# Kernel optimization log

Hardware: AMD Instinct MI355X
Metric: run time of the kernel (lower is better)

## Reference

```python
import jax, jax.numpy as jnp
import numpy as np

K = 16      # knn neighbors (init kwarg k)
EPS = 1e-5  # batch-norm eps


def setup_inputs() -> dict:
    key = jax.random.key(0)
    ks = jax.random.split(key, 4)
    B, N, C, O = 16, 2048, 16, 64
    x = jax.random.normal(ks[0], (B * N, C), dtype=jnp.float32)
    batch = jnp.repeat(jnp.arange(B, dtype=jnp.int32), N)  # sorted equal-size graphs
    W1 = jax.random.normal(ks[1], (2 * C, O), dtype=jnp.float32) * (1.0 / np.sqrt(2 * C))
    b1 = jnp.zeros((O,), jnp.float32)
    g1 = jnp.ones((O,), jnp.float32)
    be1 = jnp.zeros((O,), jnp.float32)
    Wg = jax.random.normal(ks[2], (O, 1), dtype=jnp.float32) * (1.0 / np.sqrt(O))
    bg = jnp.zeros((1,), jnp.float32)
    gg = jnp.ones((1,), jnp.float32)
    beg = jnp.zeros((1,), jnp.float32)
    return {"x": x, "batch": batch, "W1": W1, "b1": b1, "g1": g1, "be1": be1,
            "Wg": Wg, "bg": bg, "gg": gg, "beg": beg, "num_graphs": B}


def reference(x, batch, W1, b1, g1, be1, Wg, bg, gg, beg, num_graphs):
    B = int(num_graphs)
    total, C = x.shape
    N = total // B
    xb = x.reshape(B, N, C)

    # --- dynamic kNN graph in feature space (per graph in the batch) ---
    sq = jnp.sum(xb * xb, axis=-1)                                   # [B,N]
    d = sq[:, :, None] + sq[:, None, :] - 2.0 * jnp.einsum('bnc,bmc->bnm', xb, xb)
    _, idx = jax.lax.top_k(-d, K)                                    # [B,N,K], includes self (d=0)

    # --- edge features: cat([x_i, x_j - x_i]) ---
    xj = jax.vmap(lambda pts, ids: pts[ids])(xb, idx)                # [B,N,K,C]
    xi = jnp.broadcast_to(xb[:, :, None, :], xj.shape)               # [B,N,K,C]
    e = jnp.concatenate([xi, xj - xi], axis=-1)                      # [B,N,K,2C]

    # --- edge MLP: Linear -> BatchNorm(train stats) -> SiLU ---
    h = e @ W1 + b1                                                  # [B,N,K,O]
    mu = h.mean(axis=(0, 1, 2))
    var = h.var(axis=(0, 1, 2))
    h = jax.nn.silu((h - mu) / jnp.sqrt(var + EPS) * g1 + be1)

    # --- attentional aggregation: gate MLP -> softmax over k edges -> weighted sum ---
    gt = h @ Wg + bg                                                 # [B,N,K,1]
    gmu = gt.mean()
    gvar = gt.var()
    gt = jax.nn.silu((gt - gmu) / jnp.sqrt(gvar + EPS) * gg + beg)
    a = jax.nn.softmax(gt, axis=2)                                   # softmax over K per target node
    out = jnp.sum(a * h, axis=2)                                     # [B,N,O]
    return out.reshape(total, -1)
```

## Files before the change

kernel.cpp:

```cpp
#include <hip/hip_runtime.h>
#include <math.h>
#include <float.h>

#define BGRAPH 16
#define NPTS   2048
#define CDIM   16
#define ODIM   64
#define KNN    16
#define NTOT   (BGRAPH*NPTS)
#define NEDGE  (NTOT*KNN)
#define EPSBN  1e-5f
#define NBLK_E 2048
#define NPW    4

__global__ __launch_bounds__(256) void pq_kernel(
    const float* __restrict__ x, const float* __restrict__ W1,
    const float* __restrict__ b1,
    float* __restrict__ P, float* __restrict__ Q, float* __restrict__ sq) {
  int lane = threadIdx.x & 63;
  int nin  = threadIdx.x >> 6;
  int node = blockIdx.x * 4 + nin;
  __shared__ float xs[4][CDIM];
  if (threadIdx.x < 4*CDIM) {
    int n = threadIdx.x / CDIM, c = threadIdx.x % CDIM;
    xs[n][c] = x[(blockIdx.x*4 + n)*CDIM + c];
  }
  __syncthreads();
  float p = 0.f, q = b1[lane];
  #pragma unroll
  for (int c = 0; c < CDIM; ++c) {
    float xv = xs[nin][c];
    float wb = W1[(c+CDIM)*ODIM + lane];
    float wa = W1[c*ODIM + lane];
    p += xv * wb;
    q += xv * (wa - wb);
  }
  P[node*ODIM + lane] = p;
  Q[node*ODIM + lane] = q;
  if (lane == 0) {
    float s = 0.f;
    #pragma unroll
    for (int c = 0; c < CDIM; ++c) { float xv = xs[nin][c]; s += xv*xv; }
    sq[node] = s;
  }
}

#define KROWS 4
__device__ __forceinline__ unsigned long long packkey(float dv, int j) {
  unsigned ub = __float_as_uint(dv);
  ub ^= ((unsigned)((int)ub >> 31)) | 0x80000000u;
  return (((unsigned long long)ub) << 32) | (unsigned)j;
}

__global__ __launch_bounds__(256, 4) void knn_kernel(
    const float* __restrict__ x, const float* __restrict__ sq,
    int* __restrict__ idxOut) {
  __shared__ float sT16[CDIM][256];
  __shared__ unsigned long long skey[4][64];
  __shared__ int scnt[4];
  const int tid  = threadIdx.x;
  const int lane = tid & 63;
  const int w    = tid >> 6;
  const int blocksPerGraph = NPTS / KROWS;
  const int g     = blockIdx.x / blocksPerGraph;
  const int rb    = (blockIdx.x % blocksPerGraph) * KROWS;
  const int gbase = g * NPTS;
  const int r0    = rb + w;

  float tg[CDIM]; float tsq;
  {
    const float4* tp = (const float4*)(x + (size_t)(gbase + r0)*CDIM);
    float4 t0 = tp[0], t1 = tp[1], t2 = tp[2], t3 = tp[3];
    tg[0]=t0.x; tg[1]=t0.y; tg[2]=t0.z; tg[3]=t0.w;
    tg[4]=t1.x; tg[5]=t1.y; tg[6]=t1.z; tg[7]=t1.w;
    tg[8]=t2.x; tg[9]=t2.y; tg[10]=t2.z; tg[11]=t2.w;
    tg[12]=t3.x; tg[13]=t3.y; tg[14]=t3.z; tg[15]=t3.w;
    tsq = sq[gbase + r0];
  }

  float d[32];

  float4 a0, a1, a2, a3;
  {
    const float4* xp = (const float4*)(x + (size_t)(gbase + tid)*CDIM);
    a0 = xp[0]; a1 = xp[1]; a2 = xp[2]; a3 = xp[3];
  }

  for (int t = 0; t < NPTS/256; ++t) {
    __syncthreads();
    sT16[0][tid]=a0.x;  sT16[1][tid]=a0.y;  sT16[2][tid]=a0.z;  sT16[3][tid]=a0.w;
    sT16[4][tid]=a1.x;  sT16[5][tid]=a1.y;  sT16[6][tid]=a1.z;  sT16[7][tid]=a1.w;
    sT16[8][tid]=a2.x;  sT16[9][tid]=a2.y;  sT16[10][tid]=a2.z; sT16[11][tid]=a2.w;
    sT16[12][tid]=a3.x; sT16[13][tid]=a3.y; sT16[14][tid]=a3.z; sT16[15][tid]=a3.w;
    __syncthreads();
    if (t < NPTS/256 - 1) {
      const float4* xp = (const float4*)(x + (size_t)(gbase + (t+1)*256 + tid)*CDIM);
      a0 = xp[0]; a1 = xp[1]; a2 = xp[2]; a3 = xp[3];
    }

    float4 sq4 = *(const float4*)(sq + gbase + t*256 + 4*lane);
    float sqv[4] = {sq4.x, sq4.y, sq4.z, sq4.w};

    float dot[4] = {0.f,0.f,0.f,0.f};
    #pragma unroll
    for (int c = 0; c < CDIM; ++c) {
      float4 cv = *(const float4*)(&sT16[c][4*lane]);
      float cvv[4]; cvv[0]=cv.x; cvv[1]=cv.y; cvv[2]=cv.z; cvv[3]=cv.w;
      float xv = tg[c];
      #pragma unroll
      for (int rr = 0; rr < 4; ++rr)
        dot[rr] += xv * cvv[rr];
    }
    #pragma unroll
    for (int rr = 0; rr < 4; ++rr)
      d[t*4 + rr] = tsq + sqv[rr] - 2.f*dot[rr];
  }

  {
    float lmin = d[0];
    #pragma unroll
    for (int s = 1; s < 32; ++s) lmin = fminf(lmin, d[s]);

    float v = lmin;
    #pragma unroll
    for (int k = 2; k <= 64; k <<= 1) {
      #pragma unroll
      for (int j = k >> 1; j > 0; j >>= 1) {
        float o = __shfl_xor(v, j);
        bool asc   = ((lane & k) == 0);
        bool lower = ((lane & j) == 0);
        float mn = fminf(v, o), mx = fmaxf(v, o);
        v = (asc == lower) ? mn : mx;
      }
    }
    float T = __shfl(v, 15);

    if (lane == 0) scnt[w] = 0;
    #pragma unroll
    for (int s = 0; s < 32; ++s) {
      if (d[s] <= T) {
        int p = atomicAdd(&scnt[w], 1);
        if (p < 64) {
          int j = (s >> 2)*256 + 4*lane + (s & 3);
          skey[w][p] = packkey(d[s], j);
        }
      }
    }
    int M = scnt[w];
    int row = gbase + r0;

    if (M <= 64) {
      unsigned long long key = (lane < M) ? skey[w][lane] : ~0ull;
      #pragma unroll
      for (int k = 2; k <= 64; k <<= 1) {
        #pragma unroll
        for (int j = k >> 1; j > 0; j >>= 1) {
          unsigned long long o = __shfl_xor(key, j);
          bool asc   = ((lane & k) == 0);
          bool lower = ((lane & j) == 0);
          unsigned long long mn = (key < o) ? key : o;
          unsigned long long mx = (key < o) ? o : key;
          key = (asc == lower) ? mn : mx;
        }
      }
      if (lane < KNN)
        idxOut[(size_t)row*KNN + lane] = gbase + (int)(key & 0xffffffffu);
    } else {
      for (int sel = 0; sel < KNN; ++sel) {
        unsigned long long lb = ~0ull;
        #pragma unroll
        for (int s = 0; s < 32; ++s) {
          int j = (s >> 2)*256 + 4*lane + (s & 3);
          unsigned long long ks = packkey(d[s], j);
          if (ks < lb) lb = ks;
        }
        #pragma unroll
        for (int off = 32; off > 0; off >>= 1) {
          unsigned long long o = __shfl_xor(lb, off);
          if (o < lb) lb = o;
        }
        if (lane == 0)
          idxOut[(size_t)row*KNN + sel] = gbase + (int)(lb & 0xffffffffu);
        #pragma unroll
        for (int s = 0; s < 32; ++s) {
          int j = (s >> 2)*256 + 4*lane + (s & 3);
          if (packkey(d[s], j) == lb) d[s] = FLT_MAX;
        }
      }
    }
  }
}

__global__ __launch_bounds__(256) void stats1_kernel(
    const float* __restrict__ P, const float* __restrict__ Q,
    const int* __restrict__ idx, float* __restrict__ pbuf) {
  int lane = threadIdx.x & 63;
  int wid  = threadIdx.x >> 6;
  int grp  = lane >> 4;
  int p    = lane & 15;
  int gw   = blockIdx.x * 4 + wid;
  int n0 = gw * NPW;
  float4 s4  = {0.f,0.f,0.f,0.f};
  float4 ss4 = {0.f,0.f,0.f,0.f};
  #pragma unroll
  for (int ii = 0; ii < NPW; ++ii) {
    int i = n0 + ii;
    float4 q4 = *(const float4*)(Q + (size_t)i*ODIM + 4*p);
    int4 j4 = *(const int4*)(idx + (size_t)i*KNN + 4*grp);
    {
      float4 v = *(const float4*)(P + (size_t)j4.x*ODIM + 4*p);
      float hx=q4.x+v.x, hy=q4.y+v.y, hz=q4.z+v.z, hw=q4.w+v.w;
      s4.x+=hx; s4.y+=hy; s4.z+=hz; s4.w+=hw;
      ss4.x+=hx*hx; ss4.y+=hy*hy; ss4.z+=hz*hz; ss4.w+=hw*hw;
    }
    {
      float4 v = *(const float4*)(P + (size_t)j4.y*ODIM + 4*p);
      float hx=q4.x+v.x, hy=q4.y+v.y, hz=q4.z+v.z, hw=q4.w+v.w;
      s4.x+=hx; s4.y+=hy; s4.z+=hz; s4.w+=hw;
      ss4.x+=hx*hx; ss4.y+=hy*hy; ss4.z+=hz*hz; ss4.w+=hw*hw;
    }
    {
      float4 v = *(const float4*)(P + (size_t)j4.z*ODIM + 4*p);
      float hx=q4.x+v.x, hy=q4.y+v.y, hz=q4.z+v.z, hw=q4.w+v.w;
      s4.x+=hx; s4.y+=hy; s4.z+=hz; s4.w+=hw;
      ss4.x+=hx*hx; ss4.y+=hy*hy; ss4.z+=hz*hz; ss4.w+=hw*hw;
    }
    {
      float4 v = *(const float4*)(P + (size_t)j4.w*ODIM + 4*p);
      float hx=q4.x+v.x, hy=q4.y+v.y, hz=q4.z+v.z, hw=q4.w+v.w;
      s4.x+=hx; s4.y+=hy; s4.z+=hz; s4.w+=hw;
      ss4.x+=hx*hx; ss4.y+=hy*hy; ss4.z+=hz*hz; ss4.w+=hw*hw;
    }
  }
  s4.x  += __shfl_xor(s4.x,16);  s4.x  += __shfl_xor(s4.x,32);
  s4.y  += __shfl_xor(s4.y,16);  s4.y  += __shfl_xor(s4.y,32);
  s4.z  += __shfl_xor(s4.z,16);  s4.z  += __shfl_xor(s4.z,32);
  s4.w  += __shfl_xor(s4.w,16);  s4.w  += __shfl_xor(s4.w,32);
  ss4.x += __shfl_xor(ss4.x,16); ss4.x += __shfl_xor(ss4.x,32);
  ss4.y += __shfl_xor(ss4.y,16); ss4.y += __shfl_xor(ss4.y,32);
  ss4.z += __shfl_xor(ss4.z,16); ss4.z += __shfl_xor(ss4.z,32);
  ss4.w += __shfl_xor(ss4.w,16); ss4.w += __shfl_xor(ss4.w,32);
  __shared__ float ls[4][ODIM], lss[4][ODIM];
  if (grp == 0) {
    *(float4*)&ls[wid][4*p]  = s4;
    *(float4*)&lss[wid][4*p] = ss4;
  }
  __syncthreads();
  int tid = threadIdx.x;
  if (tid < ODIM) {
    float a = ls[0][tid] + ls[1][tid] + ls[2][tid] + ls[3][tid];
    pbuf[(size_t)tid*NBLK_E + blockIdx.x] = a;
  } else if (tid < 2*ODIM) {
    int o = tid - ODIM;
    float a = lss[0][o] + lss[1][o] + lss[2][o] + lss[3][o];
    pbuf[(size_t)(ODIM+o)*NBLK_E + blockIdx.x] = a;
  }
}

__global__ __launch_bounds__(64) void fin1_kernel(
    const float* __restrict__ pbuf,
    const float* __restrict__ g1, const float* __restrict__ be1,
    float* __restrict__ scale, float* __restrict__ shift) {
  int o = blockIdx.x, lane = threadIdx.x;
  const float* ps = pbuf + (size_t)o*NBLK_E;
  const float* pq = pbuf + (size_t)(ODIM+o)*NBLK_E;
  float s = 0.f, ss = 0.f;
  for (int t = lane; t < NBLK_E; t += 64) { s += ps[t]; ss += pq[t]; }
  #pragma unroll
  for (int off = 32; off > 0; off >>= 1) {
    s  += __shfl_xor(s, off);
    ss += __shfl_xor(ss, off);
  }
  if (lane == 0) {
    float mu  = s / (float)NEDGE;
    float var = ss / (float)NEDGE - mu*mu;
    float inv = 1.0f / sqrtf(var + EPSBN);
    float sc = g1[o] * inv;
    scale[o] = sc;
    shift[o] = be1[o] - mu * sc;
  }
}

__global__ __launch_bounds__(256) void stats2_kernel(
    const float* __restrict__ P, const float* __restrict__ Q,
    const int* __restrict__ idx, const float* __restrict__ scale,
    const float* __restrict__ shift, const float* __restrict__ Wg,
    const float* __restrict__ bg, float* __restrict__ gtbuf,
    float* __restrict__ gpart) {
  int lane = threadIdx.x & 63;
  int wid  = threadIdx.x >> 6;
  int grp  = lane >> 4;
  int p    = lane & 15;
  int gw   = blockIdx.x * 4 + wid;
  int n0 = gw * NPW;
  float4 sc4 = *(const float4*)(scale + 4*p);
  float4 sh4 = *(const float4*)(shift + 4*p);
  float4 wg4 = *(const float4*)(Wg + 4*p);
  float bgv = bg[0];
  float s = 0.f, ss = 0.f;
  #pragma unroll
  for (int ii = 0; ii < NPW; ++ii) {
    int i = n0 + ii;
    float4 q4 = *(const float4*)(Q + (size_t)i*ODIM + 4*p);
    int4 j4 = *(const int4*)(idx + (size_t)i*KNN + 4*grp);
    #pragma unroll
    for (int e = 0; e < 4; ++e) {
      int j = (e==0) ? j4.x : (e==1) ? j4.y : (e==2) ? j4.z : j4.w;
      float4 p4 = *(const float4*)(P + (size_t)j*ODIM + 4*p);
      float zx = (q4.x + p4.x)*sc4.x + sh4.x;
      float zy = (q4.y + p4.y)*sc4.y + sh4.y;
      float zz = (q4.z + p4.z)*sc4.z + sh4.z;
      float zw = (q4.w + p4.w)*sc4.w + sh4.w;
      float v = (zx/(1.f+expf(-zx)))*wg4.x
              + (zy/(1.f+expf(-zy)))*wg4.y
              + (zz/(1.f+expf(-zz)))*wg4.z
              + (zw/(1.f+expf(-zw)))*wg4.w;
      v += __shfl_xor(v, 1);
      v += __shfl_xor(v, 2);
      v += __shfl_xor(v, 4);
      v += __shfl_xor(v, 8);
      float gt = v + bgv;
      if (p == 0) gtbuf[(size_t)i*KNN + 4*grp + e] = gt;
      s += gt; ss += gt*gt;
    }
  }
  s  += __shfl_xor(s, 16);  s  += __shfl_xor(s, 32);
  ss += __shfl_xor(ss, 16); ss += __shfl_xor(ss, 32);
  __shared__ float pw[4], pws[4];
  if (lane == 0) { pw[wid] = s; pws[wid] = ss; }
  __syncthreads();
  if (threadIdx.x == 0) {
    gpart[2*blockIdx.x]   = pw[0]+pw[1]+pw[2]+pw[3];
    gpart[2*blockIdx.x+1] = pws[0]+pws[1]+pws[2]+pws[3];
  }
}

__global__ __launch_bounds__(256) void fin2_kernel(
    const float* __restrict__ gpart,
    const float* __restrict__ gg, const float* __restrict__ beg,
    float* __restrict__ gsc) {
  int tid = threadIdx.x;
  float s = 0.f, ss = 0.f;
  for (int t = tid; t < NBLK_E; t += 256) { s += gpart[2*t]; ss += gpart[2*t+1]; }
  __shared__ float as[256], bs[256];
  as[tid] = s; bs[tid] = ss;
  __syncthreads();
  #pragma unroll
  for (int st = 128; st > 0; st >>= 1) {
    if (tid < st) { as[tid] += as[tid+st]; bs[tid] += bs[tid+st]; }
    __syncthreads();
  }
  if (tid == 0) {
    float mu  = as[0] / (float)NEDGE;
    float var = bs[0] / (float)NEDGE - mu*mu;
    float inv = 1.f / sqrtf(var + EPSBN);
    float sg = gg[0] * inv;
    gsc[0] = sg; gsc[1] = beg[0] - mu * sg;
  }
}

__global__ __launch_bounds__(256) void final_kernel(
    const float* __restrict__ P, const float* __restrict__ Q,
    const int* __restrict__ idx, const float* __restrict__ scale,
    const float* __restrict__ shift, const float* __restrict__ gtbuf,
    const float* __restrict__ gsc, float* __restrict__ out) {
  int lane = threadIdx.x & 63;
  int wid  = threadIdx.x >> 6;
  int grp  = lane >> 4;
  int p    = lane & 15;
  int i = blockIdx.x * 4 + wid;
  float4 sc4 = *(const float4*)(scale + 4*p);
  float4 sh4 = *(const float4*)(shift + 4*p);
  float gscale = gsc[0], gshift = gsc[1];
  float4 q4 = *(const float4*)(Q + (size_t)i*ODIM + 4*p);
  int4   j4 = *(const int4*)(idx + (size_t)i*KNN + 4*grp);
  float4 g4 = *(const float4*)(gtbuf + (size_t)i*KNN + 4*grp);

  float z0 = g4.x*gscale + gshift, z1 = g4.y*gscale + gshift;
  float z2 = g4.z*gscale + gshift, z3 = g4.w*gscale + gshift;
  float gt0 = z0/(1.f+expf(-z0)), gt1 = z1/(1.f+expf(-z1));
  float gt2 = z2/(1.f+expf(-z2)), gt3 = z3/(1.f+expf(-z3));
  float m = fmaxf(fmaxf(gt0, gt1), fmaxf(gt2, gt3));
  m = fmaxf(m, __shfl_xor(m, 16));
  m = fmaxf(m, __shfl_xor(m, 32));
  float e0 = expf(gt0-m), e1 = expf(gt1-m), e2 = expf(gt2-m), e3 = expf(gt3-m);
  float se = e0+e1+e2+e3;
  se += __shfl_xor(se, 16);
  se += __shfl_xor(se, 32);
  float invs = 1.f / se;
  float a0 = e0*invs, a1 = e1*invs, a2 = e2*invs, a3 = e3*invs;

  float4 acc = {0.f,0.f,0.f,0.f};
  {
    float4 v = *(const float4*)(P + (size_t)j4.x*ODIM + 4*p);
    float zx=(q4.x+v.x)*sc4.x+sh4.x, zy=(q4.y+v.y)*sc4.y+sh4.y;
    float zz=(q4.z+v.z)*sc4.z+sh4.z, zw=(q4.w+v.w)*sc4.w+sh4.w;
    acc.x += a0*(zx/(1.f+expf(-zx))); acc.y += a0*(zy/(1.f+expf(-zy)));
    acc.z += a0*(zz/(1.f+expf(-zz))); acc.w += a0*(zw/(1.f+expf(-zw)));
  }
  {
    float4 v = *(const float4*)(P + (size_t)j4.y*ODIM + 4*p);
    float zx=(q4.x+v.x)*sc4.x+sh4.x, zy=(q4.y+v.y)*sc4.y+sh4.y;
    float zz=(q4.z+v.z)*sc4.z+sh4.z, zw=(q4.w+v.w)*sc4.w+sh4.w;
    acc.x += a1*(zx/(1.f+expf(-zx))); acc.y += a1*(zy/(1.f+expf(-zy)));
    acc.z += a1*(zz/(1.f+expf(-zz))); acc.w += a1*(zw/(1.f+expf(-zw)));
  }
  {
    float4 v = *(const float4*)(P + (size_t)j4.z*ODIM + 4*p);
    float zx=(q4.x+v.x)*sc4.x+sh4.x, zy=(q4.y+v.y)*sc4.y+sh4.y;
    float zz=(q4.z+v.z)*sc4.z+sh4.z, zw=(q4.w+v.w)*sc4.w+sh4.w;
    acc.x += a2*(zx/(1.f+expf(-zx))); acc.y += a2*(zy/(1.f+expf(-zy)));
    acc.z += a2*(zz/(1.f+expf(-zz))); acc.w += a2*(zw/(1.f+expf(-zw)));
  }
  {
    float4 v = *(const float4*)(P + (size_t)j4.w*ODIM + 4*p);
    float zx=(q4.x+v.x)*sc4.x+sh4.x, zy=(q4.y+v.y)*sc4.y+sh4.y;
    float zz=(q4.z+v.z)*sc4.z+sh4.z, zw=(q4.w+v.w)*sc4.w+sh4.w;
    acc.x += a3*(zx/(1.f+expf(-zx))); acc.y += a3*(zy/(1.f+expf(-zy)));
    acc.z += a3*(zz/(1.f+expf(-zz))); acc.w += a3*(zw/(1.f+expf(-zw)));
  }
  acc.x += __shfl_xor(acc.x,16); acc.x += __shfl_xor(acc.x,32);
  acc.y += __shfl_xor(acc.y,16); acc.y += __shfl_xor(acc.y,32);
  acc.z += __shfl_xor(acc.z,16); acc.z += __shfl_xor(acc.z,32);
  acc.w += __shfl_xor(acc.w,16); acc.w += __shfl_xor(acc.w,32);
  if (grp == 0)
    *(float4*)(out + (size_t)i*ODIM + 4*p) = acc;
}

extern "C" void kernel_launch(void* const* d_in, const int* in_sizes, int n_in,
                              void* d_out, int out_size, void* d_ws, size_t ws_size,
                              hipStream_t stream) {
  const float* x   = (const float*)d_in[0];
  const float* W1  = (const float*)d_in[2];
  const float* b1  = (const float*)d_in[3];
  const float* g1  = (const float*)d_in[4];
  const float* be1 = (const float*)d_in[5];
  const float* Wg  = (const float*)d_in[6];
  const float* bg  = (const float*)d_in[7];
  const float* gg  = (const float*)d_in[8];
  const float* beg = (const float*)d_in[9];
  float* out = (float*)d_out;

  char* ws = (char*)d_ws;
  int*   idx   = (int*)  (ws);
  float* P     = (float*)(ws + 2097152);
  float* Q     = (float*)(ws + 10485760);
  float* sq    = (float*)(ws + 18874368);
  float* pbuf  = (float*)(ws + 19005440);
  float* gpart = (float*)(ws + 20054016);
  float* gtbuf = (float*)(ws + 20070400);
  float* scale = (float*)(ws + 22167552);
  float* shift = (float*)(ws + 22167808);
  float* gsc   = (float*)(ws + 22168064);

  pq_kernel<<<NTOT/4, 256, 0, stream>>>(x, W1, b1, P, Q, sq);
  knn_kernel<<<NTOT/KROWS, 256, 0, stream>>>(x, sq, idx);
  stats1_kernel<<<NBLK_E, 256, 0, stream>>>(P, Q, idx, pbuf);
  fin1_kernel<<<ODIM, 64, 0, stream>>>(pbuf, g1, be1, scale, shift);
  stats2_kernel<<<NBLK_E, 256, 0, stream>>>(P, Q, idx, scale, shift, Wg, bg, gtbuf, gpart);
  fin2_kernel<<<1, 256, 0, stream>>>(gpart, gg, beg, gsc);
  final_kernel<<<NTOT/4, 256, 0, stream>>>(P, Q, idx, scale, shift, gtbuf, gsc, out);
}
```

Baseline: 278.7 us.

## Fuse BN stats, gate and aggregation stages into one cooperative kernel with grid syncs

Replaces the five post-kNN launches (stats1, fin1, stats2, fin2, final) with a single cooperative kernel of 1024 blocks that separates the phases with grid.sync(). Each wave handles 8 nodes, and the per-block partial reductions and finalisations run inside the same kernel. The aim is to cut launch overhead and inter-kernel gaps. In exchange it adds grid-wide barrier costs and needs all 1024 blocks to be co-resident, falling back to the old launches if the cooperative launch fails.

```diff
diff --git a/kernel.cpp b/kernel.cpp
--- a/kernel.cpp
+++ b/kernel.cpp
@@ -1,6 +1,9 @@
 #include <hip/hip_runtime.h>
+#include <hip/hip_cooperative_groups.h>
 #include <math.h>
 #include <float.h>
+
+namespace cg = cooperative_groups;
 
 #define BGRAPH 16
 #define NPTS   2048
@@ -11,6 +14,7 @@
 #define NEDGE  (NTOT*KNN)
 #define EPSBN  1e-5f
 #define NBLK_E 2048
+#define NBLKF  1024
 #define NPW    4
 
 __global__ __launch_bounds__(256) void pq_kernel(
@@ -191,6 +195,234 @@
   }
 }
 
+__global__ __launch_bounds__(256, 4) void fused_kernel(
+    const float* __restrict__ P, const float* __restrict__ Q,
+    const int* __restrict__ idx,
+    const float* __restrict__ g1, const float* __restrict__ be1,
+    const float* __restrict__ Wg, const float* __restrict__ bg,
+    const float* __restrict__ gg, const float* __restrict__ beg,
+    float* __restrict__ pbuf, float* __restrict__ gpart,
+    float* __restrict__ gtbuf, float* __restrict__ scale,
+    float* __restrict__ shift, float* __restrict__ gsc,
+    float* __restrict__ out) {
+  cg::grid_group grid = cg::this_grid();
+  const int tid  = threadIdx.x;
+  const int lane = tid & 63;
+  const int wid  = tid >> 6;
+  const int grp  = lane >> 4;
+  const int p    = lane & 15;
+  const int blk  = blockIdx.x;
+  const int nw0  = blk*32 + wid*8;
+
+  __shared__ float ls[4][ODIM], lss[4][ODIM];
+  __shared__ float ra[256], rb[256];
+  __shared__ float pw[4], pws[4];
+
+  {
+    float4 s4 = {0.f,0.f,0.f,0.f};
+    float4 ss4 = {0.f,0.f,0.f,0.f};
+    for (int ii = 0; ii < 8; ++ii) {
+      int i = nw0 + ii;
+      float4 q4 = *(const float4*)(Q + (size_t)i*ODIM + 4*p);
+      int4 j4 = *(const int4*)(idx + (size_t)i*KNN + 4*grp);
+      {
+        float4 v = *(const float4*)(P + (size_t)j4.x*ODIM + 4*p);
+        float hx=q4.x+v.x, hy=q4.y+v.y, hz=q4.z+v.z, hw=q4.w+v.w;
+        s4.x+=hx; s4.y+=hy; s4.z+=hz; s4.w+=hw;
+        ss4.x+=hx*hx; ss4.y+=hy*hy; ss4.z+=hz*hz; ss4.w+=hw*hw;
+      }
+      {
+        float4 v = *(const float4*)(P + (size_t)j4.y*ODIM + 4*p);
+        float hx=q4.x+v.x, hy=q4.y+v.y, hz=q4.z+v.z, hw=q4.w+v.w;
+        s4.x+=hx; s4.y+=hy; s4.z+=hz; s4.w+=hw;
+        ss4.x+=hx*hx; ss4.y+=hy*hy; ss4.z+=hz*hz; ss4.w+=hw*hw;
+      }
+      {
+        float4 v = *(const float4*)(P + (size_t)j4.z*ODIM + 4*p);
+        float hx=q4.x+v.x, hy=q4.y+v.y, hz=q4.z+v.z, hw=q4.w+v.w;
+        s4.x+=hx; s4.y+=hy; s4.z+=hz; s4.w+=hw;
+        ss4.x+=hx*hx; ss4.y+=hy*hy; ss4.z+=hz*hz; ss4.w+=hw*hw;
+      }
+      {
+        float4 v = *(const float4*)(P + (size_t)j4.w*ODIM + 4*p);
+        float hx=q4.x+v.x, hy=q4.y+v.y, hz=q4.z+v.z, hw=q4.w+v.w;
+        s4.x+=hx; s4.y+=hy; s4.z+=hz; s4.w+=hw;
+        ss4.x+=hx*hx; ss4.y+=hy*hy; ss4.z+=hz*hz; ss4.w+=hw*hw;
+      }
+    }
+    s4.x  += __shfl_xor(s4.x,16);  s4.x  += __shfl_xor(s4.x,32);
+    s4.y  += __shfl_xor(s4.y,16);  s4.y  += __shfl_xor(s4.y,32);
+    s4.z  += __shfl_xor(s4.z,16);  s4.z  += __shfl_xor(s4.z,32);
+    s4.w  += __shfl_xor(s4.w,16);  s4.w  += __shfl_xor(s4.w,32);
+    ss4.x += __shfl_xor(ss4.x,16); ss4.x += __shfl_xor(ss4.x,32);
+    ss4.y += __shfl_xor(ss4.y,16); ss4.y += __shfl_xor(ss4.y,32);
+    ss4.z += __shfl_xor(ss4.z,16); ss4.z += __shfl_xor(ss4.z,32);
+    ss4.w += __shfl_xor(ss4.w,16); ss4.w += __shfl_xor(ss4.w,32);
+    if (grp == 0) {
+      *(float4*)&ls[wid][4*p]  = s4;
+      *(float4*)&lss[wid][4*p] = ss4;
+    }
+    __syncthreads();
+    if (tid < ODIM) {
+      pbuf[(size_t)tid*NBLKF + blk] = ls[0][tid]+ls[1][tid]+ls[2][tid]+ls[3][tid];
+    } else if (tid < 2*ODIM) {
+      int o = tid - ODIM;
+      pbuf[(size_t)(ODIM+o)*NBLKF + blk] = lss[0][o]+lss[1][o]+lss[2][o]+lss[3][o];
+    }
+  }
+  grid.sync();
+
+  if (blk < ODIM) {
+    int o = blk;
+    float s = 0.f, ss = 0.f;
+    for (int t = tid; t < NBLKF; t += 256) {
+      s  += pbuf[(size_t)o*NBLKF + t];
+      ss += pbuf[(size_t)(ODIM+o)*NBLKF + t];
+    }
+    ra[tid] = s; rb[tid] = ss;
+    __syncthreads();
+    #pragma unroll
+    for (int st = 128; st > 0; st >>= 1) {
+      if (tid < st) { ra[tid] += ra[tid+st]; rb[tid] += rb[tid+st]; }
+      __syncthreads();
+    }
+    if (tid == 0) {
+      float mu  = ra[0] / (float)NEDGE;
+      float var = rb[0] / (float)NEDGE - mu*mu;
+      float inv = 1.0f / sqrtf(var + EPSBN);
+      float sc = g1[o] * inv;
+      scale[o] = sc;
+      shift[o] = be1[o] - mu * sc;
+    }
+  }
+  grid.sync();
+
+  {
+    float4 sc4 = *(const float4*)(scale + 4*p);
+    float4 sh4 = *(const float4*)(shift + 4*p);
+    float4 wg4 = *(const float4*)(Wg + 4*p);
+    float bgv = bg[0];
+    float s = 0.f, ss = 0.f;
+    for (int ii = 0; ii < 8; ++ii) {
+      int i = nw0 + ii;
+      float4 q4 = *(const float4*)(Q + (size_t)i*ODIM + 4*p);
+      int4 j4 = *(const int4*)(idx + (size_t)i*KNN + 4*grp);
+      #pragma unroll
+      for (int e = 0; e < 4; ++e) {
+        int j = (e==0) ? j4.x : (e==1) ? j4.y : (e==2) ? j4.z : j4.w;
+        float4 p4 = *(const float4*)(P + (size_t)j*ODIM + 4*p);
+        float zx = (q4.x + p4.x)*sc4.x + sh4.x;
+        float zy = (q4.y + p4.y)*sc4.y + sh4.y;
+        float zz = (q4.z + p4.z)*sc4.z + sh4.z;
+        float zw = (q4.w + p4.w)*sc4.w + sh4.w;
+        float v = (zx/(1.f+expf(-zx)))*wg4.x
+                + (zy/(1.f+expf(-zy)))*wg4.y
+                + (zz/(1.f+expf(-zz)))*wg4.z
+                + (zw/(1.f+expf(-zw)))*wg4.w;
+        v += __shfl_xor(v, 1);
+        v += __shfl_xor(v, 2);
+        v += __shfl_xor(v, 4);
+        v += __shfl_xor(v, 8);
+        float gt = v + bgv;
+        if (p == 0) gtbuf[(size_t)i*KNN + 4*grp + e] = gt;
+        s += gt; ss += gt*gt;
+      }
+    }
+    s  += __shfl_xor(s, 16);  s  += __shfl_xor(s, 32);
+    ss += __shfl_xor(ss, 16); ss += __shfl_xor(ss, 32);
+    if (lane == 0) { pw[wid] = s; pws[wid] = ss; }
+    __syncthreads();
+    if (tid == 0) {
+      gpart[2*blk]   = pw[0]+pw[1]+pw[2]+pw[3];
+      gpart[2*blk+1] = pws[0]+pws[1]+pws[2]+pws[3];
+    }
+  }
+  grid.sync();
+
+  if (blk == 0) {
+    float s = 0.f, ss = 0.f;
+    for (int t = tid; t < NBLKF; t += 256) { s += gpart[2*t]; ss += gpart[2*t+1]; }
+    __syncthreads();
+    ra[tid] = s; rb[tid] = ss;
+    __syncthreads();
+    #pragma unroll
+    for (int st = 128; st > 0; st >>= 1) {
+      if (tid < st) { ra[tid] += ra[tid+st]; rb[tid] += rb[tid+st]; }
+      __syncthreads();
+    }
+    if (tid == 0) {
+      float mu  = ra[0] / (float)NEDGE;
+      float var = rb[0] / (float)NEDGE - mu*mu;
+      float inv = 1.f / sqrtf(var + EPSBN);
+      float sg = gg[0] * inv;
+      gsc[0] = sg; gsc[1] = beg[0] - mu * sg;
+    }
+  }
+  grid.sync();
+
+  {
+    float4 sc4 = *(const float4*)(scale + 4*p);
+    float4 sh4 = *(const float4*)(shift + 4*p);
+    float gscale = gsc[0], gshift = gsc[1];
+    for (int ii = 0; ii < 8; ++ii) {
+      int i = nw0 + ii;
+      float4 q4 = *(const float4*)(Q + (size_t)i*ODIM + 4*p);
+      int4   j4 = *(const int4*)(idx + (size_t)i*KNN + 4*grp);
+      float4 g4 = *(const float4*)(gtbuf + (size_t)i*KNN + 4*grp);
+
+      float z0 = g4.x*gscale + gshift, z1 = g4.y*gscale + gshift;
+      float z2 = g4.z*gscale + gshift, z3 = g4.w*gscale + gshift;
+      float gt0 = z0/(1.f+expf(-z0)), gt1 = z1/(1.f+expf(-z1));
+      float gt2 = z2/(1.f+expf(-z2)), gt3 = z3/(1.f+expf(-z3));
+      float m = fmaxf(fmaxf(gt0, gt1), fmaxf(gt2, gt3));
+      m = fmaxf(m, __shfl_xor(m, 16));
+      m = fmaxf(m, __shfl_xor(m, 32));
+      float e0 = expf(gt0-m), e1 = expf(gt1-m), e2 = expf(gt2-m), e3 = expf(gt3-m);
+      float se = e0+e1+e2+e3;
+      se += __shfl_xor(se, 16);
+      se += __shfl_xor(se, 32);
+      float invs = 1.f / se;
+      float a0 = e0*invs, a1 = e1*invs, a2 = e2*invs, a3 = e3*invs;
+
+      float4 acc = {0.f,0.f,0.f,0.f};
+      {
+        float4 v = *(const float4*)(P + (size_t)j4.x*ODIM + 4*p);
+        float zx=(q4.x+v.x)*sc4.x+sh4.x, zy=(q4.y+v.y)*sc4.y+sh4.y;
+        float zz=(q4.z+v.z)*sc4.z+sh4.z, zw=(q4.w+v.w)*sc4.w+sh4.w;
+        acc.x += a0*(zx/(1.f+expf(-zx))); acc.y += a0*(zy/(1.f+expf(-zy)));
+        acc.z += a0*(zz/(1.f+expf(-zz))); acc.w += a0*(zw/(1.f+expf(-zw)));
+      }
+      {
+        float4 v = *(const float4*)(P + (size_t)j4.y*ODIM + 4*p);
+        float zx=(q4.x+v.x)*sc4.x+sh4.x, zy=(q4.y+v.y)*sc4.y+sh4.y;
+        float zz=(q4.z+v.z)*sc4.z+sh4.z, zw=(q4.w+v.w)*sc4.w+sh4.w;
+        acc.x += a1*(zx/(1.f+expf(-zx))); acc.y += a1*(zy/(1.f+expf(-zy)));
+        acc.z += a1*(zz/(1.f+expf(-zz))); acc.w += a1*(zw/(1.f+expf(-zw)));
+      }
+      {
+        float4 v = *(const float4*)(P + (size_t)j4.z*ODIM + 4*p);
+        float zx=(q4.x+v.x)*sc4.x+sh4.x, zy=(q4.y+v.y)*sc4.y+sh4.y;
+        float zz=(q4.z+v.z)*sc4.z+sh4.z, zw=(q4.w+v.w)*sc4.w+sh4.w;
+        acc.x += a2*(zx/(1.f+expf(-zx))); acc.y += a2*(zy/(1.f+expf(-zy)));
+        acc.z += a2*(zz/(1.f+expf(-zz))); acc.w += a2*(zw/(1.f+expf(-zw)));
+      }
+      {
+        float4 v = *(const float4*)(P + (size_t)j4.w*ODIM + 4*p);
+        float zx=(q4.x+v.x)*sc4.x+sh4.x, zy=(q4.y+v.y)*sc4.y+sh4.y;
+        float zz=(q4.z+v.z)*sc4.z+sh4.z, zw=(q4.w+v.w)*sc4.w+sh4.w;
+        acc.x += a3*(zx/(1.f+expf(-zx))); acc.y += a3*(zy/(1.f+expf(-zy)));
+        acc.z += a3*(zz/(1.f+expf(-zz))); acc.w += a3*(zw/(1.f+expf(-zw)));
+      }
+      acc.x += __shfl_xor(acc.x,16); acc.x += __shfl_xor(acc.x,32);
+      acc.y += __shfl_xor(acc.y,16); acc.y += __shfl_xor(acc.y,32);
+      acc.z += __shfl_xor(acc.z,16); acc.z += __shfl_xor(acc.z,32);
+      acc.w += __shfl_xor(acc.w,16); acc.w += __shfl_xor(acc.w,32);
+      if (grp == 0)
+        *(float4*)(out + (size_t)i*ODIM + 4*p) = acc;
+    }
+  }
+}
+
 __global__ __launch_bounds__(256) void stats1_kernel(
     const float* __restrict__ P, const float* __restrict__ Q,
     const int* __restrict__ idx, float* __restrict__ pbuf) {
@@ -455,9 +687,21 @@
 
   pq_kernel<<<NTOT/4, 256, 0, stream>>>(x, W1, b1, P, Q, sq);
   knn_kernel<<<NTOT/KROWS, 256, 0, stream>>>(x, sq, idx);
-  stats1_kernel<<<NBLK_E, 256, 0, stream>>>(P, Q, idx, pbuf);
-  fin1_kernel<<<ODIM, 64, 0, stream>>>(pbuf, g1, be1, scale, shift);
-  stats2_kernel<<<NBLK_E, 256, 0, stream>>>(P, Q, idx, scale, shift, Wg, bg, gtbuf, gpart);
-  fin2_kernel<<<1, 256, 0, stream>>>(gpart, gg, beg, gsc);
-  final_kernel<<<NTOT/4, 256, 0, stream>>>(P, Q, idx, scale, shift, gtbuf, gsc, out);
-}
+
+  void* args[] = {
+    (void*)&P, (void*)&Q, (void*)&idx,
+    (void*)&g1, (void*)&be1, (void*)&Wg, (void*)&bg, (void*)&gg, (void*)&beg,
+    (void*)&pbuf, (void*)&gpart, (void*)&gtbuf,
+    (void*)&scale, (void*)&shift, (void*)&gsc, (void*)&out
+  };
+  hipError_t cerr = hipLaunchCooperativeKernel(
+      reinterpret_cast<void*>(fused_kernel), dim3(NBLKF), dim3(256),
+      args, 0, stream);
+  if (cerr != hipSuccess) {
+    stats1_kernel<<<NBLK_E, 256, 0, stream>>>(P, Q, idx, pbuf);
+    fin1_kernel<<<ODIM, 64, 0, stream>>>(pbuf, g1, be1, scale, shift);
+    stats2_kernel<<<NBLK_E, 256, 0, stream>>>(P, Q, idx, scale, shift, Wg, bg, gtbuf, gpart);
+    fin2_kernel<<<1, 256, 0, stream>>>(gpart, gg, beg, gsc);
+    final_kernel<<<NTOT/4, 256, 0, stream>>>(P, Q, idx, scale, shift, gtbuf, gsc, out);
+  }
+}
```

Result: slower. 736.7 us (+164.3%).
